# Performance work log

Hardware: AMD Instinct MI355X
Metric: run time of the kernel (lower is better)

Reference implementation:

```python
import jax, jax.numpy as jnp
import numpy as np

B, L, H = 1, 2048, 2048          # batch, seq_len, hidden_size
E, N, K, R = 4096, 16, 4, 128    # intermediate, ssm_state, conv_kernel, dt_rank


def setup_inputs() -> dict:
    key = jax.random.key(0)
    ks = jax.random.split(key, 8)
    s = 0.02
    inp = {
        "hidden_states": jax.random.normal(ks[0], (B, L, H), jnp.float32),
        "in_proj_w": jax.random.normal(ks[1], (2 * E, H), jnp.float32) * s,
        "conv_w": jax.random.normal(ks[2], (E, 1, K), jnp.float32) * s,
        "conv_b": jax.random.normal(ks[3], (E,), jnp.float32) * s,
        "x_proj_w": jax.random.normal(ks[4], (R + 2 * N, E), jnp.float32) * s,
        "dt_proj_w": jax.random.normal(ks[5], (E, R), jnp.float32) * s,
        "dt_proj_b": jax.random.normal(ks[6], (E,), jnp.float32) * s,
        "A_log": jnp.broadcast_to(jnp.log(jnp.arange(1, N + 1, dtype=jnp.float32))[None, :], (E, N)).copy(),
        "D": jnp.ones((E,), jnp.float32),
        "out_proj_w": jax.random.normal(ks[7], (H, E), jnp.float32) * s,
    }
    return inp


def _mamba_mixer(hidden_states, in_proj_w, conv_w, conv_b, x_proj_w,
                 dt_proj_w, dt_proj_b, A_log, D, out_proj_w):
    # in_proj -> [B, L, 2E], split into hidden / gate
    proj = jnp.einsum('blh,eh->ble', hidden_states, in_proj_w)
    h, gate = jnp.split(proj, 2, axis=-1)            # each [B, L, E]

    # depthwise causal conv1d over time, padding K-1 on the left
    h_c = h.transpose(0, 2, 1)                       # [B, E, L]
    h_c = jax.lax.conv_general_dilated(
        h_c, conv_w, window_strides=(1,), padding=[(K - 1, 0)],
        feature_group_count=E, dimension_numbers=('NCH', 'OIH', 'NCH'))
    h_c = h_c + conv_b[None, :, None]
    h = jax.nn.silu(h_c).transpose(0, 2, 1)          # [B, L, E]

    # x_proj -> dt, B, C (input-dependent SSM params)
    ssm = jnp.einsum('ble,pe->blp', h, x_proj_w)     # [B, L, R+2N]
    dt, Bp, Cp = jnp.split(ssm, [R, R + N], axis=-1)
    dt = jax.nn.softplus(jnp.einsum('blr,er->ble', dt, dt_proj_w) + dt_proj_b)  # [B,L,E]

    A = -jnp.exp(A_log)                              # [E, N]
    dA = jnp.exp(dt[..., None] * A)                  # [B, L, E, N]
    dBu = (dt * h)[..., None] * Bp[:, :, None, :]    # [B, L, E, N]

    # selective scan: s_t = dA_t * s_{t-1} + dBu_t
    def step(s, xs):
        dA_t, dBu_t = xs
        s = s * dA_t + dBu_t
        return s, s

    s0 = jnp.zeros((h.shape[0], E, N), h.dtype)
    _, states = jax.lax.scan(step, s0, (dA.transpose(1, 0, 2, 3), dBu.transpose(1, 0, 2, 3)))
    # states: [L, B, E, N]
    y = jnp.einsum('lben,bln->ble', states, Cp)      # [B, L, E]
    y = y + h * D                                    # skip via D
    y = y * jax.nn.silu(gate)                        # gated output
    return jnp.einsum('ble,he->blh', y, out_proj_w)  # [B, L, H]


def reference(hidden_states, in_proj_w, conv_w, conv_b, x_proj_w,
              dt_proj_w, dt_proj_b, A_log, D, out_proj_w):
    return _mamba_mixer(hidden_states, in_proj_w, conv_w, conv_b, x_proj_w,
                        dt_proj_w, dt_proj_b, A_log, D, out_proj_w)
```

## Files before the change

kernel.cpp:

```cpp
#include <hip/hip_runtime.h>

#define LL 2048
#define HH 2048
#define EE 4096
#define NS 16
#define RR 128
#define CT 32
#define NC (LL / CT)
#define BM 128
#define BN 128
#define BK 64

typedef __bf16 bf16x8 __attribute__((ext_vector_type(8)));
typedef float f32x4 __attribute__((ext_vector_type(4)));

__device__ __forceinline__ unsigned short f2bf(float f) {
  union { float f; unsigned int u; } v; v.f = f;
  unsigned int r = v.u + 0x7fffu + ((v.u >> 16) & 1u);
  return (unsigned short)(r >> 16);
}

__device__ __forceinline__ float bf2f(unsigned short u) {
  union { unsigned int i; float f; } v;
  v.i = ((unsigned int)u) << 16;
  return v.f;
}

__device__ __forceinline__ void async_cp16(const unsigned short* g,
                                           unsigned short* l) {
  __builtin_amdgcn_global_load_lds(
      (const __attribute__((address_space(1))) unsigned int*)g,
      (__attribute__((address_space(3))) unsigned int*)l, 16, 0, 0);
}

__global__ void cast_bf16_k(const float* __restrict__ in,
                            unsigned short* __restrict__ out, int n4) {
  int i = blockIdx.x * blockDim.x + threadIdx.x;
  if (i >= n4) return;
  float4 v = reinterpret_cast<const float4*>(in)[i];
  ushort4 o;
  o.x = f2bf(v.x); o.y = f2bf(v.y); o.z = f2bf(v.z); o.w = f2bf(v.w);
  reinterpret_cast<ushort4*>(out)[i] = o;
}

__global__ void zero_k(float* __restrict__ p, int n4) {
  int i = blockIdx.x * blockDim.x + threadIdx.x;
  if (i >= n4) return;
  float4 z; z.x = z.y = z.z = z.w = 0.0f;
  reinterpret_cast<float4*>(p)[i] = z;
}

__global__ __launch_bounds__(256) void gemm_lds(
    const unsigned short* __restrict__ A,
    const unsigned short* __restrict__ B,
    float* __restrict__ C,
    int M, int N, int K, int tilesM, int splitk) {
  __shared__ __align__(16) unsigned short As[BM * BK];
  __shared__ __align__(16) unsigned short Bs[BN * BK];

  int bid = blockIdx.x;
  int tnInner = bid & 7;
  int rest = bid >> 3;
  int tm = rest % tilesM;
  int tnOuter = rest / tilesM;
  int tn = tnOuter * 8 + tnInner;

  int Kslice = K / splitk;
  int k_begin = blockIdx.y * Kslice;
  int k_end = k_begin + Kslice;

  int tid = threadIdx.x;
  int lane = tid & 63;
  int wave = tid >> 6;
  int wm = wave & 1, wn = wave >> 1;
  int m16 = lane & 15, quad = lane >> 4;

  const unsigned short* Ab = A + (size_t)tm * BM * K;
  const unsigned short* Bb = B + (size_t)tn * BN * K;

  int srow[4], sgcb[4];
#pragma unroll
  for (int it = 0; it < 4; ++it) {
    int blk = it * 256 + tid;
    srow[it] = blk >> 3;
    sgcb[it] = (blk & 7) ^ (srow[it] & 7);
  }
  int ldsbase = (tid & ~63) * 8;

  f32x4 acc[4][4];
#pragma unroll
  for (int i = 0; i < 4; ++i)
#pragma unroll
    for (int j = 0; j < 4; ++j)
#pragma unroll
      for (int t = 0; t < 4; ++t) acc[i][j][t] = 0.0f;

  for (int k0 = k_begin; k0 < k_end; k0 += BK) {
    __syncthreads();
#pragma unroll
    for (int it = 0; it < 4; ++it)
      async_cp16(Ab + (size_t)srow[it] * K + k0 + sgcb[it] * 8,
                 &As[it * 2048 + ldsbase]);
#pragma unroll
    for (int it = 0; it < 4; ++it)
      async_cp16(Bb + (size_t)srow[it] * K + k0 + sgcb[it] * 8,
                 &Bs[it * 2048 + ldsbase]);
    __syncthreads();
#pragma unroll
    for (int kk = 0; kk < 2; ++kk) {
      bf16x8 a[4], b[4];
#pragma unroll
      for (int i = 0; i < 4; ++i) {
        int rr = wm * 64 + i * 16 + m16;
        int cb = (kk << 2) + quad;
        a[i] = *reinterpret_cast<const bf16x8*>(
            &As[rr * BK + ((cb ^ (rr & 7)) << 3)]);
      }
#pragma unroll
      for (int j = 0; j < 4; ++j) {
        int rr = wn * 64 + j * 16 + m16;
        int cb = (kk << 2) + quad;
        b[j] = *reinterpret_cast<const bf16x8*>(
            &Bs[rr * BK + ((cb ^ (rr & 7)) << 3)]);
      }
#pragma unroll
      for (int i = 0; i < 4; ++i)
#pragma unroll
        for (int j = 0; j < 4; ++j)
          acc[i][j] =
              __builtin_amdgcn_mfma_f32_16x16x32_bf16(a[i], b[j], acc[i][j], 0, 0, 0);
    }
  }

  int rowB = tm * BM + wm * 64;
  int colB = tn * BN + wn * 64;
  if (splitk == 1) {
#pragma unroll
    for (int i = 0; i < 4; ++i)
#pragma unroll
      for (int j = 0; j < 4; ++j) {
        int col = colB + j * 16 + m16;
        int row0 = rowB + i * 16 + quad * 4;
#pragma unroll
        for (int t = 0; t < 4; ++t)
          C[(size_t)(row0 + t) * N + col] = acc[i][j][t];
      }
  } else {
#pragma unroll
    for (int i = 0; i < 4; ++i)
#pragma unroll
      for (int j = 0; j < 4; ++j) {
        int col = colB + j * 16 + m16;
        int row0 = rowB + i * 16 + quad * 4;
#pragma unroll
        for (int t = 0; t < 4; ++t)
          atomicAdd(&C[(size_t)(row0 + t) * N + col], acc[i][j][t]);
      }
  }
}

__global__ __launch_bounds__(256) void gemm_bt(
    const unsigned short* __restrict__ A,
    const unsigned short* __restrict__ B,
    float* __restrict__ C,
    int M, int N, int K, int tilesN, int splitk) {
  int bid = blockIdx.x;
  int groupSize = 8 * tilesN;
  int g = bid / groupSize, r = bid % groupSize;
  int tm = g * 8 + (r & 7);
  int tn = r >> 3;

  int Kslice = K / splitk;
  int k_begin = blockIdx.y * Kslice;
  int k_end = k_begin + Kslice;

  int tid = threadIdx.x;
  int wave = tid >> 6, lane = tid & 63;
  int wm = wave & 1, wn = wave >> 1;
  int m16 = lane & 15, quad = lane >> 4;
  int rowBase = tm * 64 + wm * 32;
  int colBase = tn * 128 + wn * 64;

  const unsigned short* a0p = A + (size_t)(rowBase + m16) * K + quad * 8;
  const unsigned short* a1p = A + (size_t)(rowBase + 16 + m16) * K + quad * 8;
  const unsigned short* bp[4];
  bool bok[4];
#pragma unroll
  for (int j = 0; j < 4; ++j) {
    int col = colBase + j * 16 + m16;
    bok[j] = (col < N);
    bp[j] = B + (size_t)(bok[j] ? col : 0) * K + quad * 8;
  }

  f32x4 acc[2][4];
#pragma unroll
  for (int i = 0; i < 2; ++i)
#pragma unroll
    for (int j = 0; j < 4; ++j)
#pragma unroll
      for (int t = 0; t < 4; ++t) acc[i][j][t] = 0.0f;

  bf16x8 zero8;
#pragma unroll
  for (int t = 0; t < 8; ++t) zero8[t] = (__bf16)0.0f;

  for (int k = k_begin; k < k_end; k += 32) {
    bf16x8 a0 = *reinterpret_cast<const bf16x8*>(a0p + k);
    bf16x8 a1 = *reinterpret_cast<const bf16x8*>(a1p + k);
    bf16x8 b[4];
#pragma unroll
    for (int j = 0; j < 4; ++j)
      b[j] = bok[j] ? *reinterpret_cast<const bf16x8*>(bp[j] + k) : zero8;
#pragma unroll
    for (int j = 0; j < 4; ++j) {
      acc[0][j] = __builtin_amdgcn_mfma_f32_16x16x32_bf16(a0, b[j], acc[0][j], 0, 0, 0);
      acc[1][j] = __builtin_amdgcn_mfma_f32_16x16x32_bf16(a1, b[j], acc[1][j], 0, 0, 0);
    }
  }

#pragma unroll
  for (int i = 0; i < 2; ++i)
#pragma unroll
    for (int j = 0; j < 4; ++j) {
      int col = colBase + j * 16 + m16;
      if (col >= N) continue;
      int row0 = rowBase + i * 16 + quad * 4;
      if (splitk == 1) {
#pragma unroll
        for (int t = 0; t < 4; ++t)
          C[(size_t)(row0 + t) * N + col] = acc[i][j][t];
      } else {
#pragma unroll
        for (int t = 0; t < 4; ++t)
          atomicAdd(&C[(size_t)(row0 + t) * N + col], acc[i][j][t]);
      }
    }
}

__global__ __launch_bounds__(256) void conv_silu_k(
    const float* __restrict__ proj, const float* __restrict__ cw,
    const float* __restrict__ cb, unsigned short* __restrict__ hb) {
  int e = blockIdx.x * 256 + threadIdx.x;
  int l0 = blockIdx.y * 16;
  float w0 = cw[e * 4 + 0], w1 = cw[e * 4 + 1];
  float w2 = cw[e * 4 + 2], w3 = cw[e * 4 + 3];
  float bias = cb[e];
  float xm3 = (l0 >= 3) ? proj[(size_t)(l0 - 3) * (2 * EE) + e] : 0.0f;
  float xm2 = (l0 >= 2) ? proj[(size_t)(l0 - 2) * (2 * EE) + e] : 0.0f;
  float xm1 = (l0 >= 1) ? proj[(size_t)(l0 - 1) * (2 * EE) + e] : 0.0f;
#pragma unroll
  for (int t = 0; t < 16; ++t) {
    int l = l0 + t;
    float x0 = proj[(size_t)l * (2 * EE) + e];
    float acc = bias + w0 * xm3 + w1 * xm2 + w2 * xm1 + w3 * x0;
    float s = acc / (1.0f + __expf(-acc));
    hb[(size_t)l * EE + e] = f2bf(s);
    xm3 = xm2; xm2 = xm1; xm1 = x0;
  }
}

__global__ void dtcast_k(const float* __restrict__ ssm,
                         unsigned short* __restrict__ dtin, int n) {
  int i = blockIdx.x * blockDim.x + threadIdx.x;
  if (i >= n) return;
  int l = i >> 7, r = i & 127;
  dtin[i] = f2bf(ssm[l * 160 + r]);
}

__global__ void softplus_k(float* __restrict__ dt, const float* __restrict__ db,
                           int n) {
  int i = blockIdx.x * blockDim.x + threadIdx.x;
  if (i >= n) return;
  float x = dt[i] + db[i & (EE - 1)];
  dt[i] = (x > 20.0f) ? x : log1pf(__expf(x));
}

__global__ __launch_bounds__(256) void scan_partA(
    const float* __restrict__ dt, const unsigned short* __restrict__ hb,
    const float* __restrict__ ssm, const float* __restrict__ A_log,
    float* __restrict__ P, float* __restrict__ S) {
  int e = blockIdx.y * 256 + threadIdx.x;
  int c = blockIdx.x;
  float Aa[16];
#pragma unroll
  for (int q = 0; q < 4; ++q) {
    float4 a = reinterpret_cast<const float4*>(&A_log[(size_t)e * NS])[q];
    Aa[q * 4 + 0] = -__expf(a.x);
    Aa[q * 4 + 1] = -__expf(a.y);
    Aa[q * 4 + 2] = -__expf(a.z);
    Aa[q * 4 + 3] = -__expf(a.w);
  }
  float s[16], p[16];
#pragma unroll
  for (int n = 0; n < 16; ++n) { s[n] = 0.0f; p[n] = 1.0f; }
  int l0 = c * CT;
#pragma unroll 2
  for (int t = 0; t < CT; ++t) {
    int l = l0 + t;
    size_t o = (size_t)l * EE + e;
    float dtv = dt[o];
    float hv = bf2f(hb[o]);
    float Bv[16];
#pragma unroll
    for (int q = 0; q < 4; ++q)
      *reinterpret_cast<float4*>(&Bv[q * 4]) =
          reinterpret_cast<const float4*>(&ssm[(size_t)l * 160 + 128])[q];
    float z = dtv * hv;
#pragma unroll
    for (int n = 0; n < 16; ++n) {
      float dA = __expf(dtv * Aa[n]);
      s[n] = s[n] * dA + z * Bv[n];
      p[n] *= dA;
    }
  }
  size_t base = ((size_t)c * EE + e) * NS;
#pragma unroll
  for (int q = 0; q < 4; ++q) {
    reinterpret_cast<float4*>(&P[base])[q] = *reinterpret_cast<float4*>(&p[q * 4]);
    reinterpret_cast<float4*>(&S[base])[q] = *reinterpret_cast<float4*>(&s[q * 4]);
  }
}

__global__ __launch_bounds__(256) void scan_chunkB(
    const float* __restrict__ P, float* __restrict__ S) {
  int gidx = blockIdx.x * 256 + threadIdx.x;
  float s = 0.0f;
  float pv = P[gidx], sv = S[gidx];
  for (int c = 0; c < NC; ++c) {
    float pn = 0.0f, sn = 0.0f;
    if (c + 1 < NC) {
      size_t i2 = (size_t)(c + 1) * (EE * NS) + gidx;
      pn = P[i2];
      sn = S[i2];
    }
    float s_next = s * pv + sv;
    S[(size_t)c * (EE * NS) + gidx] = s;
    s = s_next;
    pv = pn; sv = sn;
  }
}

__global__ __launch_bounds__(256) void scan_partC(
    const float* __restrict__ dt, const unsigned short* __restrict__ hb,
    const float* __restrict__ ssm, const float* __restrict__ A_log,
    const float* __restrict__ Dp, const float* __restrict__ proj,
    const float* __restrict__ Sinit, unsigned short* __restrict__ yb) {
  int e = blockIdx.y * 256 + threadIdx.x;
  int c = blockIdx.x;
  float Aa[16];
#pragma unroll
  for (int q = 0; q < 4; ++q) {
    float4 a = reinterpret_cast<const float4*>(&A_log[(size_t)e * NS])[q];
    Aa[q * 4 + 0] = -__expf(a.x);
    Aa[q * 4 + 1] = -__expf(a.y);
    Aa[q * 4 + 2] = -__expf(a.z);
    Aa[q * 4 + 3] = -__expf(a.w);
  }
  float Dv = Dp[e];
  float s[16];
  size_t base = ((size_t)c * EE + e) * NS;
#pragma unroll
  for (int q = 0; q < 4; ++q)
    *reinterpret_cast<float4*>(&s[q * 4]) =
        reinterpret_cast<const float4*>(&Sinit[base])[q];
  int l0 = c * CT;
#pragma unroll 2
  for (int t = 0; t < CT; ++t) {
    int l = l0 + t;
    size_t o = (size_t)l * EE + e;
    float dtv = dt[o];
    float hv = bf2f(hb[o]);
    float Bv[16], Cv[16];
#pragma unroll
    for (int q = 0; q < 4; ++q) {
      *reinterpret_cast<float4*>(&Bv[q * 4]) =
          reinterpret_cast<const float4*>(&ssm[(size_t)l * 160 + 128])[q];
      *reinterpret_cast<float4*>(&Cv[q * 4]) =
          reinterpret_cast<const float4*>(&ssm[(size_t)l * 160 + 144])[q];
    }
    float z = dtv * hv;
    float y = 0.0f;
#pragma unroll
    for (int n = 0; n < 16; ++n) {
      float dA = __expf(dtv * Aa[n]);
      s[n] = s[n] * dA + z * Bv[n];
      y += s[n] * Cv[n];
    }
    float gv = proj[(size_t)l * 2 * EE + EE + e];
    float yv = (y + hv * Dv) * (gv / (1.0f + __expf(-gv)));
    yb[o] = f2bf(yv);
  }
}

extern "C" void kernel_launch(void* const* d_in, const int* in_sizes, int n_in,
                              void* d_out, int out_size, void* d_ws, size_t ws_size,
                              hipStream_t stream) {
  const float* hs   = (const float*)d_in[0];
  const float* w1   = (const float*)d_in[1];
  const float* cw   = (const float*)d_in[2];
  const float* cb   = (const float*)d_in[3];
  const float* xw   = (const float*)d_in[4];
  const float* dtw  = (const float*)d_in[5];
  const float* dtb  = (const float*)d_in[6];
  const float* Alog = (const float*)d_in[7];
  const float* Dp   = (const float*)d_in[8];
  const float* ow   = (const float*)d_in[9];
  float* out = (float*)d_out;

  char* ws = (char*)d_ws;
  size_t off = 0;
  auto alloc = [&](size_t b) {
    char* p = ws + off;
    off += (b + 255) & ~(size_t)255;
    return p;
  };
  float* proj = (float*)alloc((size_t)LL * 2 * EE * 4);
  unsigned short* hb = (unsigned short*)alloc((size_t)LL * EE * 2);
  float* dtf  = (float*)alloc((size_t)LL * EE * 4);
  unsigned short* w1b = (unsigned short*)dtf;
  unsigned short* hsb = (unsigned short*)alloc((size_t)LL * HH * 2);
  unsigned short* yb  = (unsigned short*)alloc((size_t)LL * EE * 2);
  unsigned short* owb = (unsigned short*)alloc((size_t)HH * EE * 2);
  unsigned short* xwb = (unsigned short*)alloc((size_t)160 * EE * 2);
  float* ssm = (float*)alloc((size_t)LL * 160 * 4);
  unsigned short* dtin = (unsigned short*)alloc((size_t)LL * RR * 2);
  unsigned short* dtwb = (unsigned short*)alloc((size_t)EE * RR * 2);
  float* Pbuf = (float*)alloc((size_t)NC * EE * NS * 4);
  float* Sbuf = (float*)alloc((size_t)NC * EE * NS * 4);

  auto cast = [&](const float* in, unsigned short* o, int nelem) {
    int n4 = nelem / 4;
    cast_bf16_k<<<(n4 + 255) / 256, 256, 0, stream>>>(in, o, n4);
  };
  cast(hs, hsb, LL * HH);
  cast(w1, w1b, 2 * EE * HH);
  cast(xw, xwb, 160 * EE);
  cast(dtw, dtwb, EE * RR);
  cast(ow, owb, HH * EE);
  zero_k<<<(LL * 160 / 4 + 255) / 256, 256, 0, stream>>>(ssm, LL * 160 / 4);
  zero_k<<<(LL * HH / 4 + 255) / 256, 256, 0, stream>>>(out, LL * HH / 4);

  auto gemmL = [&](const unsigned short* A, const unsigned short* Bm, float* Cm,
                   int M, int N, int K, int splitk) {
    int tilesN = N / BN, tilesM = M / BM;
    gemm_lds<<<dim3(tilesM * tilesN, splitk), 256, 0, stream>>>(
        A, Bm, Cm, M, N, K, tilesM, splitk);
  };

  gemmL(hsb, w1b, proj, LL, 2 * EE, HH, 1);
  conv_silu_k<<<dim3(EE / 256, LL / 16), 256, 0, stream>>>(proj, cw, cb, hb);
  {
    int tilesN = (160 + 127) / 128, tilesM = LL / 64;
    gemm_bt<<<dim3(tilesM * tilesN, 8), 256, 0, stream>>>(
        hb, xwb, ssm, LL, 160, EE, tilesN, 8);
  }
  dtcast_k<<<(LL * RR + 255) / 256, 256, 0, stream>>>(ssm, dtin, LL * RR);
  gemmL(dtin, dtwb, dtf, LL, EE, RR, 1);
  softplus_k<<<(LL * EE + 255) / 256, 256, 0, stream>>>(dtf, dtb, LL * EE);
  scan_partA<<<dim3(NC, EE / 256), 256, 0, stream>>>(dtf, hb, ssm, Alog, Pbuf, Sbuf);
  scan_chunkB<<<EE * NS / 256, 256, 0, stream>>>(Pbuf, Sbuf);
  scan_partC<<<dim3(NC, EE / 256), 256, 0, stream>>>(dtf, hb, ssm, Alog, Dp, proj,
                                                     Sbuf, yb);
  gemmL(yb, owb, out, LL, HH, EE, 2);
}
```

Baseline: 473.1 us.

## Fuse gate SiLU and softplus into GEMM epilogues, enlarge scan chunks

The in_proj GEMM epilogue now splits its output: the hidden half is written as fp32 and the gate half is written as bf16 after SiLU. This removes the full fp32 gate store and the re-read plus SiLU inside the scan. The dt_proj GEMM applies the bias and softplus in its epilogue, so the separate softplus pass over the LLxEE buffer is gone. Scan chunk length is doubled, which halves the number of chunks handled in the inter-chunk pass but leaves fewer parallel blocks in the chunk kernels. Storing the gate in bf16 adds rounding error.

New measurement: 493.6 us. +4.3%, slower.

```diff
diff --git a/kernel.cpp b/kernel.cpp
--- a/kernel.cpp
+++ b/kernel.cpp
@@ -5,7 +5,7 @@
 #define EE 4096
 #define NS 16
 #define RR 128
-#define CT 32
+#define CT 64
 #define NC (LL / CT)
 #define BM 128
 #define BN 128
@@ -54,7 +54,9 @@
     const unsigned short* __restrict__ A,
     const unsigned short* __restrict__ B,
     float* __restrict__ C,
-    int M, int N, int K, int tilesM, int splitk) {
+    int M, int N, int K, int tilesM, int splitk, int epi,
+    const float* __restrict__ bias, float* __restrict__ auxF,
+    unsigned short* __restrict__ auxB) {
   __shared__ __align__(16) unsigned short As[BM * BK];
   __shared__ __align__(16) unsigned short Bs[BN * BK];
 
@@ -134,7 +136,7 @@
 
   int rowB = tm * BM + wm * 64;
   int colB = tn * BN + wn * 64;
-  if (splitk == 1) {
+  if (epi == 0) {
 #pragma unroll
     for (int i = 0; i < 4; ++i)
 #pragma unroll
@@ -145,7 +147,7 @@
         for (int t = 0; t < 4; ++t)
           C[(size_t)(row0 + t) * N + col] = acc[i][j][t];
       }
-  } else {
+  } else if (epi == 1) {
 #pragma unroll
     for (int i = 0; i < 4; ++i)
 #pragma unroll
@@ -155,6 +157,43 @@
 #pragma unroll
         for (int t = 0; t < 4; ++t)
           atomicAdd(&C[(size_t)(row0 + t) * N + col], acc[i][j][t]);
+      }
+  } else if (epi == 2) {
+    bool isGate = (colB >= EE);
+#pragma unroll
+    for (int i = 0; i < 4; ++i)
+#pragma unroll
+      for (int j = 0; j < 4; ++j) {
+        int col = colB + j * 16 + m16;
+        int row0 = rowB + i * 16 + quad * 4;
+        if (!isGate) {
+#pragma unroll
+          for (int t = 0; t < 4; ++t)
+            auxF[(size_t)(row0 + t) * EE + col] = acc[i][j][t];
+        } else {
+          int cg = col - EE;
+#pragma unroll
+          for (int t = 0; t < 4; ++t) {
+            float v = acc[i][j][t];
+            float s = v / (1.0f + __expf(-v));
+            auxB[(size_t)(row0 + t) * EE + cg] = f2bf(s);
+          }
+        }
+      }
+  } else {
+#pragma unroll
+    for (int i = 0; i < 4; ++i)
+#pragma unroll
+      for (int j = 0; j < 4; ++j) {
+        int col = colB + j * 16 + m16;
+        float bv = bias[col];
+        int row0 = rowB + i * 16 + quad * 4;
+#pragma unroll
+        for (int t = 0; t < 4; ++t) {
+          float x = acc[i][j][t] + bv;
+          C[(size_t)(row0 + t) * N + col] =
+              (x > 20.0f) ? x : log1pf(__expf(x));
+        }
       }
   }
 }
@@ -238,20 +277,20 @@
 }
 
 __global__ __launch_bounds__(256) void conv_silu_k(
-    const float* __restrict__ proj, const float* __restrict__ cw,
+    const float* __restrict__ projh, const float* __restrict__ cw,
     const float* __restrict__ cb, unsigned short* __restrict__ hb) {
   int e = blockIdx.x * 256 + threadIdx.x;
   int l0 = blockIdx.y * 16;
   float w0 = cw[e * 4 + 0], w1 = cw[e * 4 + 1];
   float w2 = cw[e * 4 + 2], w3 = cw[e * 4 + 3];
   float bias = cb[e];
-  float xm3 = (l0 >= 3) ? proj[(size_t)(l0 - 3) * (2 * EE) + e] : 0.0f;
-  float xm2 = (l0 >= 2) ? proj[(size_t)(l0 - 2) * (2 * EE) + e] : 0.0f;
-  float xm1 = (l0 >= 1) ? proj[(size_t)(l0 - 1) * (2 * EE) + e] : 0.0f;
+  float xm3 = (l0 >= 3) ? projh[(size_t)(l0 - 3) * EE + e] : 0.0f;
+  float xm2 = (l0 >= 2) ? projh[(size_t)(l0 - 2) * EE + e] : 0.0f;
+  float xm1 = (l0 >= 1) ? projh[(size_t)(l0 - 1) * EE + e] : 0.0f;
 #pragma unroll
   for (int t = 0; t < 16; ++t) {
     int l = l0 + t;
-    float x0 = proj[(size_t)l * (2 * EE) + e];
+    float x0 = projh[(size_t)l * EE + e];
     float acc = bias + w0 * xm3 + w1 * xm2 + w2 * xm1 + w3 * x0;
     float s = acc / (1.0f + __expf(-acc));
     hb[(size_t)l * EE + e] = f2bf(s);
@@ -265,14 +304,6 @@
   if (i >= n) return;
   int l = i >> 7, r = i & 127;
   dtin[i] = f2bf(ssm[l * 160 + r]);
-}
-
-__global__ void softplus_k(float* __restrict__ dt, const float* __restrict__ db,
-                           int n) {
-  int i = blockIdx.x * blockDim.x + threadIdx.x;
-  if (i >= n) return;
-  float x = dt[i] + db[i & (EE - 1)];
-  dt[i] = (x > 20.0f) ? x : log1pf(__expf(x));
 }
 
 __global__ __launch_bounds__(256) void scan_partA(
@@ -343,7 +374,7 @@
 __global__ __launch_bounds__(256) void scan_partC(
     const float* __restrict__ dt, const unsigned short* __restrict__ hb,
     const float* __restrict__ ssm, const float* __restrict__ A_log,
-    const float* __restrict__ Dp, const float* __restrict__ proj,
+    const float* __restrict__ Dp, const unsigned short* __restrict__ sg,
     const float* __restrict__ Sinit, unsigned short* __restrict__ yb) {
   int e = blockIdx.y * 256 + threadIdx.x;
   int c = blockIdx.x;
@@ -386,8 +417,8 @@
       s[n] = s[n] * dA + z * Bv[n];
       y += s[n] * Cv[n];
     }
-    float gv = proj[(size_t)l * 2 * EE + EE + e];
-    float yv = (y + hv * Dv) * (gv / (1.0f + __expf(-gv)));
+    float gv = bf2f(sg[o]);
+    float yv = (y + hv * Dv) * gv;
     yb[o] = f2bf(yv);
   }
 }
@@ -414,7 +445,8 @@
     off += (b + 255) & ~(size_t)255;
     return p;
   };
-  float* proj = (float*)alloc((size_t)LL * 2 * EE * 4);
+  float* projh = (float*)alloc((size_t)LL * EE * 4);
+  unsigned short* sg = (unsigned short*)alloc((size_t)LL * EE * 2);
   unsigned short* hb = (unsigned short*)alloc((size_t)LL * EE * 2);
   float* dtf  = (float*)alloc((size_t)LL * EE * 4);
   unsigned short* w1b = (unsigned short*)dtf;
@@ -440,26 +472,30 @@
   zero_k<<<(LL * 160 / 4 + 255) / 256, 256, 0, stream>>>(ssm, LL * 160 / 4);
   zero_k<<<(LL * HH / 4 + 255) / 256, 256, 0, stream>>>(out, LL * HH / 4);
 
-  auto gemmL = [&](const unsigned short* A, const unsigned short* Bm, float* Cm,
-                   int M, int N, int K, int splitk) {
-    int tilesN = N / BN, tilesM = M / BM;
-    gemm_lds<<<dim3(tilesM * tilesN, splitk), 256, 0, stream>>>(
-        A, Bm, Cm, M, N, K, tilesM, splitk);
-  };
-
-  gemmL(hsb, w1b, proj, LL, 2 * EE, HH, 1);
-  conv_silu_k<<<dim3(EE / 256, LL / 16), 256, 0, stream>>>(proj, cw, cb, hb);
+  {
+    int tilesN = (2 * EE) / BN, tilesM = LL / BM;
+    gemm_lds<<<dim3(tilesM * tilesN, 1), 256, 0, stream>>>(
+        hsb, w1b, nullptr, LL, 2 * EE, HH, tilesM, 1, 2, nullptr, projh, sg);
+  }
+  conv_silu_k<<<dim3(EE / 256, LL / 16), 256, 0, stream>>>(projh, cw, cb, hb);
   {
     int tilesN = (160 + 127) / 128, tilesM = LL / 64;
     gemm_bt<<<dim3(tilesM * tilesN, 8), 256, 0, stream>>>(
         hb, xwb, ssm, LL, 160, EE, tilesN, 8);
   }
   dtcast_k<<<(LL * RR + 255) / 256, 256, 0, stream>>>(ssm, dtin, LL * RR);
-  gemmL(dtin, dtwb, dtf, LL, EE, RR, 1);
-  softplus_k<<<(LL * EE + 255) / 256, 256, 0, stream>>>(dtf, dtb, LL * EE);
+  {
+    int tilesN = EE / BN, tilesM = LL / BM;
+    gemm_lds<<<dim3(tilesM * tilesN, 1), 256, 0, stream>>>(
+        dtin, dtwb, dtf, LL, EE, RR, tilesM, 1, 3, dtb, nullptr, nullptr);
+  }
   scan_partA<<<dim3(NC, EE / 256), 256, 0, stream>>>(dtf, hb, ssm, Alog, Pbuf, Sbuf);
   scan_chunkB<<<EE * NS / 256, 256, 0, stream>>>(Pbuf, Sbuf);
-  scan_partC<<<dim3(NC, EE / 256), 256, 0, stream>>>(dtf, hb, ssm, Alog, Dp, proj,
+  scan_partC<<<dim3(NC, EE / 256), 256, 0, stream>>>(dtf, hb, ssm, Alog, Dp, sg,
                                                      Sbuf, yb);
-  gemmL(yb, owb, out, LL, HH, EE, 2);
-}
+  {
+    int tilesN = HH / BN, tilesM = LL / BM;
+    gemm_lds<<<dim3(tilesM * tilesN, 2), 256, 0, stream>>>(
+        yb, owb, out, LL, HH, EE, tilesM, 2, 1, nullptr, nullptr, nullptr);
+  }
+}
```
